# Optimization experiments

Hardware: AMD Instinct MI355X
Metric: run time of the kernel (lower is better)

The kernel has to match this reference:

```python
import jax, jax.numpy as jnp
import numpy as np

VOCAB = 50257
HID = 1024
MAXLEN = 64


def setup_inputs() -> dict:
    key = jax.random.key(0)
    ks = jax.random.split(key, 12)
    s = 1.0 / np.sqrt(HID)
    return {
        "input": jax.random.randint(ks[0], (1,), 0, VOCAB),
        "hidden": jax.random.normal(ks[1], (1, 1, HID), jnp.float32),
        "enc_outputs": jax.random.normal(ks[2], (MAXLEN, HID), jnp.float32),
        "emb": jax.random.normal(ks[3], (VOCAB, HID), jnp.float32),
        "attn_W": jax.random.uniform(ks[4], (MAXLEN, 2 * HID), jnp.float32, -s, s),
        "attn_b": jnp.zeros((MAXLEN,), jnp.float32),
        "comb_W": jax.random.uniform(ks[5], (HID, 2 * HID), jnp.float32, -s, s),
        "comb_b": jnp.zeros((HID,), jnp.float32),
        "gru_Wih": jax.random.uniform(ks[6], (3 * HID, HID), jnp.float32, -s, s),
        "gru_Whh": jax.random.uniform(ks[7], (3 * HID, HID), jnp.float32, -s, s),
        "gru_bih": jnp.zeros((3 * HID,), jnp.float32),
        "gru_bhh": jnp.zeros((3 * HID,), jnp.float32),
        "out_W": jax.random.uniform(ks[8], (VOCAB, HID), jnp.float32, -s, s),
        "out_b": jnp.zeros((VOCAB,), jnp.float32),
    }


def reference(input, hidden, enc_outputs, emb, attn_W, attn_b, comb_W, comb_b,
              gru_Wih, gru_Whh, gru_bih, gru_bhh, out_W, out_b):
    # embedded: [1, HID] (dropout is identity in eval / p=0)
    embedded = emb[input[0]][None, :]
    h = hidden[0]  # [1, HID]
    # attention over encoder positions
    cat_eh = jnp.concatenate([embedded, h], axis=1)           # [1, 2H]
    attn_weights = jax.nn.softmax(cat_eh @ attn_W.T + attn_b, axis=1)  # [1, MAXLEN]
    attn_applied = attn_weights @ enc_outputs                  # [1, HID]
    # combine
    x = jnp.concatenate([embedded, attn_applied], axis=1)      # [1, 2H]
    x = jax.nn.relu(x @ comb_W.T + comb_b)                     # [1, HID]
    # single GRU step (PyTorch gate order: r, z, n)
    gi = x @ gru_Wih.T + gru_bih                                # [1, 3H]
    gh = h @ gru_Whh.T + gru_bhh                                # [1, 3H]
    i_r, i_z, i_n = jnp.split(gi, 3, axis=1)
    h_r, h_z, h_n = jnp.split(gh, 3, axis=1)
    r = jax.nn.sigmoid(i_r + h_r)
    z = jax.nn.sigmoid(i_z + h_z)
    n = jnp.tanh(i_n + r * h_n)
    h_new = (1.0 - z) * n + z * h                               # [1, HID]
    # output projection + log-softmax
    logp = jax.nn.log_softmax(h_new @ out_W.T + out_b, axis=1)  # [1, VOCAB]
    return logp, h_new[None, :, :], attn_weights
```

## Files before the change

### kernel.cpp

```cpp
#include <hip/hip_runtime.h>
#include <hip/hip_bf16.h>

#define VOCAB 50257
#define HID   1024
#define MAXLEN 64

__device__ __forceinline__ float dot4(float4 a, float4 b){
  return a.x*b.x + a.y*b.y + a.z*b.z + a.w*b.w;
}
__device__ __forceinline__ float dot4f(float4 a, const float* v){
  return a.x*v[0] + a.y*v[1] + a.z*v[2] + a.w*v[3];
}

__global__ __launch_bounds__(256) void k_attn_scores(
    const int* tok_p, const float* hidden, const float* emb,
    const float* attn_W, const float* attn_b, float* ws_scores){
  int b = blockIdx.x, t = threadIdx.x;
  int tok = min(max(tok_p[0], 0), VOCAB-1);
  const float4* wv = (const float4*)(attn_W + (size_t)b*2048);
  const float4* ef = (const float4*)(emb + (size_t)tok*HID);
  const float4* hf = (const float4*)hidden;
  float acc = dot4(wv[t], ef[t]) + dot4(wv[256+t], hf[t]);
  #pragma unroll
  for (int k=32;k>=1;k>>=1) acc += __shfl_xor(acc,k);
  __shared__ float red[4];
  if ((t&63)==0) red[t>>6] = acc;
  __syncthreads();
  if (t==0) ws_scores[b] = red[0]+red[1]+red[2]+red[3] + attn_b[b];
}

__global__ __launch_bounds__(1024) void k_softmax_attn(
    const float* ws_scores, const float* enc,
    float* ws_attn, float* out_attn){
  int t = threadIdx.x;
  __shared__ float sw[MAXLEN];
  if (t < 64) {
    float s = ws_scores[t];
    float m = s;
    #pragma unroll
    for (int k=32;k>=1;k>>=1) m = fmaxf(m, __shfl_xor(m,k));
    float e = expf(s-m), d = e;
    #pragma unroll
    for (int k=32;k>=1;k>>=1) d += __shfl_xor(d,k);
    float w = e/d;
    sw[t] = w;
    out_attn[t] = w;
  }
  __syncthreads();
  float acc = 0.f;
  #pragma unroll 8
  for (int p=0;p<MAXLEN;p++) acc += sw[p]*enc[p*HID + t];
  ws_attn[t] = acc;
}

__global__ __launch_bounds__(256) void k_combine(
    const int* tok_p, const float* ws_attn, const float* emb,
    const float* comb_W, const float* comb_b, float* ws_x){
  int wave = threadIdx.x>>6, lane = threadIdx.x&63;
  int row = blockIdx.x*4 + wave;
  int tok = min(max(tok_p[0], 0), VOCAB-1);
  const float4* wrow = (const float4*)(comb_W + (size_t)row*2048);
  const float4* erow = (const float4*)(emb + (size_t)tok*HID);
  const float4* av   = (const float4*)ws_attn;
  float acc = 0.f;
  #pragma unroll
  for (int c=0;c<4;c++) acc += dot4(wrow[c*64+lane],     erow[c*64+lane]);
  #pragma unroll
  for (int c=0;c<4;c++) acc += dot4(wrow[256+c*64+lane], av[c*64+lane]);
  #pragma unroll
  for (int k=32;k>=1;k>>=1) acc += __shfl_xor(acc,k);
  if (lane==0) ws_x[row] = fmaxf(acc + comb_b[row], 0.f);
}

__global__ __launch_bounds__(256) void k_gru_mv(
    const float* ws_x, const float* hidden,
    const float* Wih, const float* Whh,
    const float* bih, const float* bhh,
    float* ws_gi, float* ws_gh){
  int wave = threadIdx.x>>6, lane = threadIdx.x&63;
  int g = blockIdx.x*4 + wave;
  bool ih = g < 3*HID;
  int row = ih ? g : g - 3*HID;
  const float* W = ih ? Wih : Whh;
  const float4* wrow = (const float4*)(W + (size_t)row*HID);
  const float4* vec  = ih ? (const float4*)ws_x : (const float4*)hidden;
  float acc = 0.f;
  #pragma unroll
  for (int c=0;c<4;c++) acc += dot4(wrow[c*64+lane], vec[c*64+lane]);
  #pragma unroll
  for (int k=32;k>=1;k>>=1) acc += __shfl_xor(acc,k);
  if (lane==0) {
    if (ih) ws_gi[row] = acc + bih[row];
    else    ws_gh[row] = acc + bhh[row];
  }
}

__global__ __launch_bounds__(1024) void k_gru_gate(
    const float* gi, const float* gh, const float* hidden,
    float* ws_h, float* out_h){
  int t = threadIdx.x;
  float r = 1.f/(1.f+expf(-(gi[t]        + gh[t])));
  float z = 1.f/(1.f+expf(-(gi[HID+t]    + gh[HID+t])));
  float n = tanhf(gi[2*HID+t] + r*gh[2*HID+t]);
  float h = hidden[t];
  float hn = (1.f-z)*n + z*h;
  ws_h[t] = hn;
  out_h[t] = hn;
}

__global__ __launch_bounds__(256) void k_logits(
    const float* wsh, const float* out_W, const float* out_b,
    float* out_logits, float* ws_stats){
  int wave = threadIdx.x>>6, lane = threadIdx.x&63;
  int gw = blockIdx.x*4 + wave;
  float hv[16];
  #pragma unroll
  for (int c=0;c<4;c++)
    #pragma unroll
    for (int j=0;j<4;j++) hv[c*4+j] = wsh[c*256 + lane*4 + j];
  float m = -INFINITY, s = 0.f;
  for (int row = gw; row < VOCAB; row += 8192) {
    const float4* wrow = (const float4*)(out_W + (size_t)row*HID);
    float acc = 0.f;
    #pragma unroll
    for (int c=0;c<4;c++) acc += dot4f(wrow[c*64+lane], hv + c*4);
    #pragma unroll
    for (int k=32;k>=1;k>>=1) acc += __shfl_xor(acc,k);
    if (lane==0) {
      float logit = acc + out_b[row];
      out_logits[row] = logit;
      if (logit > m) { s = s*expf(m-logit) + 1.f; m = logit; }
      else s += expf(logit-m);
    }
  }
  __shared__ float sm[4], ss[4];
  if (lane==0){ sm[wave]=m; ss[wave]=s; }
  __syncthreads();
  if (threadIdx.x==0) {
    float M = fmaxf(fmaxf(sm[0],sm[1]),fmaxf(sm[2],sm[3]));
    float S = ss[0]*expf(sm[0]-M)+ss[1]*expf(sm[1]-M)
            + ss[2]*expf(sm[2]-M)+ss[3]*expf(sm[3]-M);
    ws_stats[blockIdx.x*2]   = M;
    ws_stats[blockIdx.x*2+1] = S;
  }
}

__global__ __launch_bounds__(256) void k_lse(const float* ws_stats, float* ws_lse){
  int t = threadIdx.x;
  float m = -INFINITY, s = 0.f;
  for (int i=t;i<2048;i+=256){
    float mi = ws_stats[2*i], si = ws_stats[2*i+1];
    float M = fmaxf(m,mi);
    s = s*expf(m-M) + si*expf(mi-M);
    m = M;
  }
  #pragma unroll
  for (int k=32;k>=1;k>>=1){
    float mo = __shfl_xor(m,k), so = __shfl_xor(s,k);
    float M = fmaxf(m,mo);
    s = s*expf(m-M) + so*expf(mo-M);
    m = M;
  }
  __shared__ float sm[4], ss[4];
  if ((t&63)==0){ sm[t>>6]=m; ss[t>>6]=s; }
  __syncthreads();
  if (t==0){
    float M = fmaxf(fmaxf(sm[0],sm[1]),fmaxf(sm[2],sm[3]));
    float S = ss[0]*expf(sm[0]-M)+ss[1]*expf(sm[1]-M)
            + ss[2]*expf(sm[2]-M)+ss[3]*expf(sm[3]-M);
    ws_lse[0] = M + logf(S);
  }
}

__global__ __launch_bounds__(256) void k_logp(float* out_logits, const float* ws_lse){
  int i = blockIdx.x*256 + threadIdx.x;
  if (i < VOCAB) out_logits[i] = out_logits[i] - ws_lse[0];
}

extern "C" void kernel_launch(void* const* d_in, const int* in_sizes, int n_in,
                              void* d_out, int out_size, void* d_ws, size_t ws_size,
                              hipStream_t stream) {
  const int*   tok    = (const int*)d_in[0];
  const float* hidden = (const float*)d_in[1];
  const float* enc    = (const float*)d_in[2];
  const float* emb    = (const float*)d_in[3];
  const float* attn_W = (const float*)d_in[4];
  const float* attn_b = (const float*)d_in[5];
  const float* comb_W = (const float*)d_in[6];
  const float* comb_b = (const float*)d_in[7];
  const float* Wih    = (const float*)d_in[8];
  const float* Whh    = (const float*)d_in[9];
  const float* bih    = (const float*)d_in[10];
  const float* bhh    = (const float*)d_in[11];
  const float* out_W  = (const float*)d_in[12];
  const float* out_b  = (const float*)d_in[13];

  float* out      = (float*)d_out;
  float* out_logp = out;
  float* out_h    = out + VOCAB;
  float* out_attn = out + VOCAB + HID;

  float* ws        = (float*)d_ws;
  float* ws_scores = ws;
  float* ws_attn   = ws + 128;
  float* ws_x      = ws + 1152;
  float* ws_gi     = ws + 2176;
  float* ws_gh     = ws + 5248;
  float* ws_h      = ws + 8320;
  float* ws_stats  = ws + 9344;
  float* ws_lse    = ws + 13440;

  k_attn_scores <<<64,   256, 0, stream>>>(tok, hidden, emb, attn_W, attn_b, ws_scores);
  k_softmax_attn<<<1,    1024,0, stream>>>(ws_scores, enc, ws_attn, out_attn);
  k_combine     <<<256,  256, 0, stream>>>(tok, ws_attn, emb, comb_W, comb_b, ws_x);
  k_gru_mv      <<<1536, 256, 0, stream>>>(ws_x, hidden, Wih, Whh, bih, bhh, ws_gi, ws_gh);
  k_gru_gate    <<<1,    1024,0, stream>>>(ws_gi, ws_gh, hidden, ws_h, out_h);
  k_logits      <<<2048, 256, 0, stream>>>(ws_h, out_W, out_b, out_logp, ws_stats);
  k_lse         <<<1,    256, 0, stream>>>(ws_stats, ws_lse);
  k_logp        <<<197,  256, 0, stream>>>(out_logp, ws_lse);
}
```

Baseline: 424.8 us.

## Fuse attention softmax into combine, GRU gates into matvec, LSE into logp

```diff
diff --git a/kernel.cpp b/kernel.cpp
--- a/kernel.cpp
+++ b/kernel.cpp
@@ -29,39 +29,38 @@
   if (t==0) ws_scores[b] = red[0]+red[1]+red[2]+red[3] + attn_b[b];
 }
 
-__global__ __launch_bounds__(1024) void k_softmax_attn(
-    const float* ws_scores, const float* enc,
-    float* ws_attn, float* out_attn){
-  int t = threadIdx.x;
+__global__ __launch_bounds__(256) void k_combine_fused(
+    const int* tok_p, const float* ws_scores, const float* enc,
+    const float* emb, const float* comb_W, const float* comb_b,
+    float* ws_x, float* out_attn){
+  int t = threadIdx.x, wave = t>>6, lane = t&63;
   __shared__ float sw[MAXLEN];
-  if (t < 64) {
-    float s = ws_scores[t];
-    float m = s;
-    #pragma unroll
-    for (int k=32;k>=1;k>>=1) m = fmaxf(m, __shfl_xor(m,k));
-    float e = expf(s-m), d = e;
-    #pragma unroll
-    for (int k=32;k>=1;k>>=1) d += __shfl_xor(d,k);
-    float w = e/d;
-    sw[t] = w;
-    out_attn[t] = w;
-  }
-  __syncthreads();
-  float acc = 0.f;
+  __shared__ float sa[HID];
+  float s = ws_scores[lane];
+  float m = s;
+  #pragma unroll
+  for (int k=32;k>=1;k>>=1) m = fmaxf(m, __shfl_xor(m,k));
+  float e = expf(s-m), d = e;
+  #pragma unroll
+  for (int k=32;k>=1;k>>=1) d += __shfl_xor(d,k);
+  float w = e/d;
+  if (wave==0) sw[lane] = w;
+  if (blockIdx.x==0 && wave==0) out_attn[lane] = w;
+  __syncthreads();
+  float4 a4 = make_float4(0.f,0.f,0.f,0.f);
   #pragma unroll 8
-  for (int p=0;p<MAXLEN;p++) acc += sw[p]*enc[p*HID + t];
-  ws_attn[t] = acc;
-}
-
-__global__ __launch_bounds__(256) void k_combine(
-    const int* tok_p, const float* ws_attn, const float* emb,
-    const float* comb_W, const float* comb_b, float* ws_x){
-  int wave = threadIdx.x>>6, lane = threadIdx.x&63;
+  for (int p=0;p<MAXLEN;p++){
+    float wp = sw[p];
+    float4 ev = *(const float4*)(enc + (size_t)p*HID + t*4);
+    a4.x += wp*ev.x; a4.y += wp*ev.y; a4.z += wp*ev.z; a4.w += wp*ev.w;
+  }
+  *(float4*)(sa + t*4) = a4;
+  __syncthreads();
   int row = blockIdx.x*4 + wave;
   int tok = min(max(tok_p[0], 0), VOCAB-1);
   const float4* wrow = (const float4*)(comb_W + (size_t)row*2048);
   const float4* erow = (const float4*)(emb + (size_t)tok*HID);
-  const float4* av   = (const float4*)ws_attn;
+  const float4* av   = (const float4*)sa;
   float acc = 0.f;
   #pragma unroll
   for (int c=0;c<4;c++) acc += dot4(wrow[c*64+lane],     erow[c*64+lane]);
@@ -72,40 +71,41 @@
   if (lane==0) ws_x[row] = fmaxf(acc + comb_b[row], 0.f);
 }
 
-__global__ __launch_bounds__(256) void k_gru_mv(
+__global__ __launch_bounds__(256) void k_gru_fused(
     const float* ws_x, const float* hidden,
     const float* Wih, const float* Whh,
     const float* bih, const float* bhh,
-    float* ws_gi, float* ws_gh){
-  int wave = threadIdx.x>>6, lane = threadIdx.x&63;
-  int g = blockIdx.x*4 + wave;
-  bool ih = g < 3*HID;
-  int row = ih ? g : g - 3*HID;
-  const float* W = ih ? Wih : Whh;
-  const float4* wrow = (const float4*)(W + (size_t)row*HID);
-  const float4* vec  = ih ? (const float4*)ws_x : (const float4*)hidden;
-  float acc = 0.f;
-  #pragma unroll
-  for (int c=0;c<4;c++) acc += dot4(wrow[c*64+lane], vec[c*64+lane]);
-  #pragma unroll
-  for (int k=32;k>=1;k>>=1) acc += __shfl_xor(acc,k);
-  if (lane==0) {
-    if (ih) ws_gi[row] = acc + bih[row];
-    else    ws_gh[row] = acc + bhh[row];
-  }
-}
-
-__global__ __launch_bounds__(1024) void k_gru_gate(
-    const float* gi, const float* gh, const float* hidden,
     float* ws_h, float* out_h){
-  int t = threadIdx.x;
-  float r = 1.f/(1.f+expf(-(gi[t]        + gh[t])));
-  float z = 1.f/(1.f+expf(-(gi[HID+t]    + gh[HID+t])));
-  float n = tanhf(gi[2*HID+t] + r*gh[2*HID+t]);
-  float h = hidden[t];
-  float hn = (1.f-z)*n + z*h;
-  ws_h[t] = hn;
-  out_h[t] = hn;
+  int t = threadIdx.x, wave = t>>6, lane = t&63;
+  __shared__ float part[2][6];
+  for (int idx = wave; idx < 12; idx += 4){
+    int u  = (idx >= 6) ? 1 : 0;
+    int g  = idx - u*6;
+    int hi = blockIdx.x*2 + u;
+    bool ih = (g < 3);
+    int gg = ih ? g : g-3;
+    const float*  W = ih ? Wih : Whh;
+    const float*  b = ih ? bih : bhh;
+    const float4* vec  = ih ? (const float4*)ws_x : (const float4*)hidden;
+    const float4* wrow = (const float4*)(W + ((size_t)gg*HID + hi)*HID);
+    float acc = 0.f;
+    #pragma unroll
+    for (int c=0;c<4;c++) acc += dot4(wrow[c*64+lane], vec[c*64+lane]);
+    #pragma unroll
+    for (int k=32;k>=1;k>>=1) acc += __shfl_xor(acc,k);
+    if (lane==0) part[u][g] = acc + b[gg*HID + hi];
+  }
+  __syncthreads();
+  if (t < 2){
+    int hi = blockIdx.x*2 + t;
+    float r = 1.f/(1.f+expf(-(part[t][0] + part[t][3])));
+    float z = 1.f/(1.f+expf(-(part[t][1] + part[t][4])));
+    float n = tanhf(part[t][2] + r*part[t][5]);
+    float h = hidden[hi];
+    float hn = (1.f-z)*n + z*h;
+    ws_h[hi]  = hn;
+    out_h[hi] = hn;
+  }
 }
 
 __global__ __launch_bounds__(256) void k_logits(
@@ -145,9 +145,11 @@
   }
 }
 
-__global__ __launch_bounds__(256) void k_lse(const float* ws_stats, float* ws_lse){
+__global__ __launch_bounds__(256) void k_logp_fused(
+    const float* ws_stats, float* out_logits){
   int t = threadIdx.x;
   float m = -INFINITY, s = 0.f;
+  #pragma unroll
   for (int i=t;i<2048;i+=256){
     float mi = ws_stats[2*i], si = ws_stats[2*i+1];
     float M = fmaxf(m,mi);
@@ -162,19 +164,18 @@
     m = M;
   }
   __shared__ float sm[4], ss[4];
+  __shared__ float slse;
   if ((t&63)==0){ sm[t>>6]=m; ss[t>>6]=s; }
   __syncthreads();
   if (t==0){
     float M = fmaxf(fmaxf(sm[0],sm[1]),fmaxf(sm[2],sm[3]));
     float S = ss[0]*expf(sm[0]-M)+ss[1]*expf(sm[1]-M)
             + ss[2]*expf(sm[2]-M)+ss[3]*expf(sm[3]-M);
-    ws_lse[0] = M + logf(S);
-  }
-}
-
-__global__ __launch_bounds__(256) void k_logp(float* out_logits, const float* ws_lse){
-  int i = blockIdx.x*256 + threadIdx.x;
-  if (i < VOCAB) out_logits[i] = out_logits[i] - ws_lse[0];
+    slse = M + logf(S);
+  }
+  __syncthreads();
+  int i = blockIdx.x*256 + t;
+  if (i < VOCAB) out_logits[i] -= slse;
 }
 
 extern "C" void kernel_launch(void* const* d_in, const int* in_sizes, int n_in,
@@ -202,20 +203,13 @@
 
   float* ws        = (float*)d_ws;
   float* ws_scores = ws;
-  float* ws_attn   = ws + 128;
-  float* ws_x      = ws + 1152;
-  float* ws_gi     = ws + 2176;
-  float* ws_gh     = ws + 5248;
-  float* ws_h      = ws + 8320;
-  float* ws_stats  = ws + 9344;
-  float* ws_lse    = ws + 13440;
-
-  k_attn_scores <<<64,   256, 0, stream>>>(tok, hidden, emb, attn_W, attn_b, ws_scores);
-  k_softmax_attn<<<1,    1024,0, stream>>>(ws_scores, enc, ws_attn, out_attn);
-  k_combine     <<<256,  256, 0, stream>>>(tok, ws_attn, emb, comb_W, comb_b, ws_x);
-  k_gru_mv      <<<1536, 256, 0, stream>>>(ws_x, hidden, Wih, Whh, bih, bhh, ws_gi, ws_gh);
-  k_gru_gate    <<<1,    1024,0, stream>>>(ws_gi, ws_gh, hidden, ws_h, out_h);
-  k_logits      <<<2048, 256, 0, stream>>>(ws_h, out_W, out_b, out_logp, ws_stats);
-  k_lse         <<<1,    256, 0, stream>>>(ws_stats, ws_lse);
-  k_logp        <<<197,  256, 0, stream>>>(out_logp, ws_lse);
-}
+  float* ws_x      = ws + 128;
+  float* ws_h      = ws + 1280;
+  float* ws_stats  = ws + 2432;
+
+  k_attn_scores  <<<64,   256, 0, stream>>>(tok, hidden, emb, attn_W, attn_b, ws_scores);
+  k_combine_fused<<<256,  256, 0, stream>>>(tok, ws_scores, enc, emb, comb_W, comb_b, ws_x, out_attn);
+  k_gru_fused    <<<512,  256, 0, stream>>>(ws_x, hidden, Wih, Whh, bih, bhh, ws_h, out_h);
+  k_logits       <<<2048, 256, 0, stream>>>(ws_h, out_W, out_b, out_logp, ws_stats);
+  k_logp_fused   <<<197,  256, 0, stream>>>(ws_stats, out_logp);
+}
```

After: 422.9 us. About the same (-0.5%).
